# Kernel tuning notes

Measured on AMD Instinct MI355X. Metric: run time of the kernel, lower is better.

The kernel has to match this reference:

```python
import jax, jax.numpy as jnp
import numpy as np

N = 50000
E = 800000
NODE_DIM = 128
EDGE_DIM = 128
HIDDEN_DIM = 256


def setup_inputs() -> dict:
    key = jax.random.key(0)
    k_x, k_ei, k_ea, k_w1, k_b1, k_w2, k_b2 = jax.random.split(key, 7)
    x = jax.random.normal(k_x, (N, NODE_DIM), dtype=jnp.float32)
    edge_index = jax.random.randint(k_ei, (2, E), 0, N, dtype=jnp.int64)
    edge_attr = jax.random.normal(k_ea, (E, EDGE_DIM), dtype=jnp.float32)
    u = jnp.zeros((1, NODE_DIM), dtype=jnp.float32)
    batch = jnp.zeros((N,), dtype=jnp.int64)
    in_dim = NODE_DIM + EDGE_DIM
    # torch Linear: y = x @ W.T + b, W shaped [out, in]
    W1 = jax.random.normal(k_w1, (HIDDEN_DIM, in_dim), dtype=jnp.float32) / np.sqrt(in_dim)
    b1 = jax.random.normal(k_b1, (HIDDEN_DIM,), dtype=jnp.float32) * 0.01
    W2 = jax.random.normal(k_w2, (NODE_DIM, HIDDEN_DIM), dtype=jnp.float32) / np.sqrt(HIDDEN_DIM)
    b2 = jax.random.normal(k_b2, (NODE_DIM,), dtype=jnp.float32) * 0.01
    return {"x": x, "edge_index": edge_index, "edge_attr": edge_attr, "u": u,
            "batch": batch, "W1": W1, "b1": b1, "W2": W2, "b2": b2}


def reference(x, edge_index, edge_attr, u, batch, W1, b1, W2, b2):
    # row, col = edge_index; scatter_add edge features into destination nodes
    col = edge_index[1]
    agg = jax.ops.segment_sum(edge_attr, col, num_segments=x.shape[0])  # [N, EDGE_DIM]
    out = jnp.concatenate([x, agg], axis=1)                              # [N, NODE_DIM+EDGE_DIM]
    h = jax.nn.relu(out @ W1.T + b1)                                     # [N, HIDDEN_DIM]
    return h @ W2.T + b2                                                 # [N, NODE_DIM]
```

## Files before the change

### kernel.cpp

```cpp
#include <hip/hip_runtime.h>

typedef __bf16 bf16;
typedef __attribute__((ext_vector_type(8))) __bf16 bf16x8;
typedef __attribute__((ext_vector_type(4))) __bf16 bf16x4;
typedef __attribute__((ext_vector_type(4))) float f32x4;

#define ND 128
#define IN_DIM 256
#define HD 256
#define OUT_D 128
#define BCAP 128

__global__ __launch_bounds__(256) void prep_kernel(const float* __restrict__ W1,
                                                   const float* __restrict__ W2,
                                                   bf16* __restrict__ W1b,
                                                   bf16* __restrict__ W2b,
                                                   int* __restrict__ cnt, int N) {
    int i = blockIdx.x * 256 + threadIdx.x;
    if (i < HD * IN_DIM) W1b[i] = (bf16)W1[i];
    if (i < OUT_D * HD) W2b[i] = (bf16)W2[i];
    if (i < N) cnt[i] = 0;
}

__global__ __launch_bounds__(256) void bucket_kernel(const int* __restrict__ col,
                                                     int* __restrict__ cnt,
                                                     int* __restrict__ bucket, int E) {
    int e = blockIdx.x * blockDim.x + threadIdx.x;
    if (e < E) {
        int c = col[e];
        int slot = atomicAdd(&cnt[c], 1);
        if (slot < BCAP) bucket[(size_t)c * BCAP + slot] = e;
    }
}

__global__ __launch_bounds__(256) void gather_kernel(const float4* __restrict__ ea,
                                                     const float4* __restrict__ x,
                                                     const int* __restrict__ cnt,
                                                     const int* __restrict__ bucket,
                                                     bf16* __restrict__ rowb, int N) {
    int wave = (int)((blockIdx.x * (long long)blockDim.x + threadIdx.x) >> 6);
    int lane = threadIdx.x & 63;
    if (wave >= N) return;
    const int q = lane & 31;
    const int s = lane >> 5;

    if (s == 0) {
        float4 xv = x[wave * 32 + q];
        bf16x4 o;
        o[0] = (bf16)xv.x; o[1] = (bf16)xv.y; o[2] = (bf16)xv.z; o[3] = (bf16)xv.w;
        *(bf16x4*)(rowb + (size_t)wave * IN_DIM + q * 4) = o;
    }

    int deg = cnt[wave];
    if (deg > BCAP) deg = BCAP;
    const int* bl = bucket + (size_t)wave * BCAP;
    float4 acc = make_float4(0.f, 0.f, 0.f, 0.f);

    for (int chunk = 0; chunk < deg; chunk += 64) {
        const int c64 = min(64, deg - chunk);
        int myid = (chunk + lane < deg) ? bl[chunk + lane] : 0;
        int j0 = s, j1 = s + 2;
        int id0 = __shfl(myid, j0);
        int id1 = __shfl(myid, j1);
        float4 v0, v1;
        if (j0 < c64) v0 = ea[(id0 << 5) + q];
        if (j1 < c64) v1 = ea[(id1 << 5) + q];
        while (j0 < c64) {
            float4 c0 = v0;
            bool h1 = (j1 < c64);
            float4 c1;
            if (h1) c1 = v1;
            int j2 = j0 + 4, j3 = j1 + 4;
            int id2 = __shfl(myid, j2 & 63);
            int id3 = __shfl(myid, j3 & 63);
            if (j2 < c64) v0 = ea[(id2 << 5) + q];
            if (j3 < c64) v1 = ea[(id3 << 5) + q];
            acc.x += c0.x; acc.y += c0.y; acc.z += c0.z; acc.w += c0.w;
            if (h1) { acc.x += c1.x; acc.y += c1.y; acc.z += c1.z; acc.w += c1.w; }
            j0 = j2; j1 = j3;
        }
    }

    acc.x += __shfl_xor(acc.x, 32);
    acc.y += __shfl_xor(acc.y, 32);
    acc.z += __shfl_xor(acc.z, 32);
    acc.w += __shfl_xor(acc.w, 32);
    if (s == 0) {
        bf16x4 o;
        o[0] = (bf16)acc.x; o[1] = (bf16)acc.y; o[2] = (bf16)acc.z; o[3] = (bf16)acc.w;
        *(bf16x4*)(rowb + (size_t)wave * IN_DIM + ND + q * 4) = o;
    }
}

__device__ __forceinline__ int hswz(int row, int col) {
    int c = col >> 3, sub = col & 7;
    return row * HD + (((c ^ (row & 7)) << 3) | sub);
}

__global__ __launch_bounds__(256) void mlp_kernel(const bf16* __restrict__ rowb,
                                                  const bf16* __restrict__ W1b,
                                                  const float* __restrict__ b1,
                                                  const bf16* __restrict__ W2b,
                                                  const float* __restrict__ b2,
                                                  float* __restrict__ y, int N) {
    __shared__ bf16 hl[4][32 * HD];
    const int w = threadIdx.x >> 6;
    const int lane = threadIdx.x & 63;
    const int l15 = lane & 15;
    const int g = lane >> 4;
    const int nb0 = blockIdx.x * 128 + w * 32;
    const int nb1 = nb0 + 16;
    const bool val0 = nb0 < N, val1 = nb1 < N;
    const int nbe0 = val0 ? nb0 : 0;
    const int nbe1 = val1 ? nb1 : 0;

    bf16x8 a0[8], a1[8];
#pragma unroll
    for (int k0 = 0; k0 < 8; k0++) {
        a0[k0] = *(const bf16x8*)(rowb + (size_t)(nbe0 + l15) * IN_DIM + k0 * 32 + g * 8);
        a1[k0] = *(const bf16x8*)(rowb + (size_t)(nbe1 + l15) * IN_DIM + k0 * 32 + g * 8);
    }

#pragma unroll
    for (int jt = 0; jt < 16; jt++) {
        f32x4 acc0 = {0.f, 0.f, 0.f, 0.f}, acc1 = {0.f, 0.f, 0.f, 0.f};
#pragma unroll
        for (int k0 = 0; k0 < 8; k0++) {
            bf16x8 b = *(const bf16x8*)(W1b + (size_t)(jt * 16 + l15) * IN_DIM + k0 * 32 + g * 8);
            acc0 = __builtin_amdgcn_mfma_f32_16x16x32_bf16(a0[k0], b, acc0, 0, 0, 0);
            acc1 = __builtin_amdgcn_mfma_f32_16x16x32_bf16(a1[k0], b, acc1, 0, 0, 0);
        }
        float bj = b1[jt * 16 + l15];
        int colj = jt * 16 + l15;
#pragma unroll
        for (int r = 0; r < 4; r++) {
            int row = g * 4 + r;
            float v0 = acc0[r] + bj;
            float v1 = acc1[r] + bj;
            hl[w][hswz(row, colj)]      = (bf16)(v0 > 0.f ? v0 : 0.f);
            hl[w][hswz(row + 16, colj)] = (bf16)(v1 > 0.f ? v1 : 0.f);
        }
    }
    __syncthreads();

    bf16x8 h0[8], h1[8];
#pragma unroll
    for (int k0 = 0; k0 < 8; k0++) {
        h0[k0] = *(const bf16x8*)&hl[w][hswz(l15,      k0 * 32 + g * 8)];
        h1[k0] = *(const bf16x8*)&hl[w][hswz(l15 + 16, k0 * 32 + g * 8)];
    }

#pragma unroll
    for (int jt = 0; jt < 8; jt++) {
        f32x4 acc0 = {0.f, 0.f, 0.f, 0.f}, acc1 = {0.f, 0.f, 0.f, 0.f};
#pragma unroll
        for (int k0 = 0; k0 < 8; k0++) {
            bf16x8 b = *(const bf16x8*)(W2b + (size_t)(jt * 16 + l15) * HD + k0 * 32 + g * 8);
            acc0 = __builtin_amdgcn_mfma_f32_16x16x32_bf16(h0[k0], b, acc0, 0, 0, 0);
            acc1 = __builtin_amdgcn_mfma_f32_16x16x32_bf16(h1[k0], b, acc1, 0, 0, 0);
        }
        float bm = b2[jt * 16 + l15];
#pragma unroll
        for (int r = 0; r < 4; r++) {
            if (val0) y[(size_t)(nb0 + g * 4 + r) * OUT_D + jt * 16 + l15] = acc0[r] + bm;
            if (val1) y[(size_t)(nb1 + g * 4 + r) * OUT_D + jt * 16 + l15] = acc1[r] + bm;
        }
    }
}

extern "C" void kernel_launch(void* const* d_in, const int* in_sizes, int n_in,
                              void* d_out, int out_size, void* d_ws, size_t ws_size,
                              hipStream_t stream) {
    const float* x  = (const float*)d_in[0];
    const int* edge_index = (const int*)d_in[1];
    const float* ea = (const float*)d_in[2];
    const float* W1 = (const float*)d_in[5];
    const float* b1 = (const float*)d_in[6];
    const float* W2 = (const float*)d_in[7];
    const float* b2 = (const float*)d_in[8];
    float* y = (float*)d_out;

    const int E = in_sizes[1] / 2;
    const int N = in_sizes[0] / ND;
    const int* col = edge_index + E;

    char* ws = (char*)d_ws;
    size_t off = 0;
    bf16* rowb = (bf16*)(ws + off); off += (size_t)N * IN_DIM * sizeof(bf16);
    bf16* W1b  = (bf16*)(ws + off); off += (size_t)HD * IN_DIM * sizeof(bf16);
    bf16* W2b  = (bf16*)(ws + off); off += (size_t)OUT_D * HD * sizeof(bf16);
    int* cnt    = (int*)(ws + off); off += (size_t)N * sizeof(int);
    int* bucket = (int*)(ws + off); off += (size_t)N * BCAP * sizeof(int);

    prep_kernel<<<(HD * IN_DIM + 255) / 256, 256, 0, stream>>>(W1, W2, W1b, W2b, cnt, N);
    bucket_kernel<<<(E + 255) / 256, 256, 0, stream>>>(col, cnt, bucket, E);

    {
        long long threads = (long long)N * 64;
        int blocks = (int)((threads + 255) / 256);
        gather_kernel<<<blocks, 256, 0, stream>>>((const float4*)ea, (const float4*)x,
                                                  cnt, bucket, rowb, N);
    }

    mlp_kernel<<<(N + 127) / 128, 256, 0, stream>>>(rowb, W1b, b1, W2b, b2, y, N);
}
```

Measured before the change: 205.8 us.

## Fuse edge gather and MLP into one kernel with shared-memory row tile

New measurement: 244.5 us. +18.8%, slower.

```diff
diff --git a/kernel.cpp b/kernel.cpp
--- a/kernel.cpp
+++ b/kernel.cpp
@@ -10,6 +10,11 @@
 #define HD 256
 #define OUT_D 128
 #define BCAP 128
+
+__device__ __forceinline__ int hswz(int row, int col) {
+    int c = col >> 3, sub = col & 7;
+    return row * 256 + (((c ^ (row & 7)) << 3) | sub);
+}
 
 __global__ __launch_bounds__(256) void prep_kernel(const float* __restrict__ W1,
                                                    const float* __restrict__ W2,
@@ -33,137 +38,117 @@
     }
 }
 
-__global__ __launch_bounds__(256) void gather_kernel(const float4* __restrict__ ea,
-                                                     const float4* __restrict__ x,
-                                                     const int* __restrict__ cnt,
-                                                     const int* __restrict__ bucket,
-                                                     bf16* __restrict__ rowb, int N) {
-    int wave = (int)((blockIdx.x * (long long)blockDim.x + threadIdx.x) >> 6);
-    int lane = threadIdx.x & 63;
-    if (wave >= N) return;
+__global__ __launch_bounds__(256) void fused_kernel(const float4* __restrict__ ea,
+                                                    const float4* __restrict__ x,
+                                                    const int* __restrict__ cnt,
+                                                    const int* __restrict__ bucket,
+                                                    const bf16* __restrict__ W1b,
+                                                    const float* __restrict__ b1,
+                                                    const bf16* __restrict__ W2b,
+                                                    const float* __restrict__ b2,
+                                                    float* __restrict__ y, int N) {
+    __shared__ bf16 tile[64 * 256];
+    const int w = threadIdx.x >> 6;
+    const int lane = threadIdx.x & 63;
     const int q = lane & 31;
     const int s = lane >> 5;
+    const int l15 = lane & 15;
+    const int g = lane >> 4;
+    const int nb = blockIdx.x * 64 + w * 16;
+    const bool valid = nb < N;
 
-    if (s == 0) {
-        float4 xv = x[wave * 32 + q];
-        bf16x4 o;
-        o[0] = (bf16)xv.x; o[1] = (bf16)xv.y; o[2] = (bf16)xv.z; o[3] = (bf16)xv.w;
-        *(bf16x4*)(rowb + (size_t)wave * IN_DIM + q * 4) = o;
-    }
-
-    int deg = cnt[wave];
-    if (deg > BCAP) deg = BCAP;
-    const int* bl = bucket + (size_t)wave * BCAP;
-    float4 acc = make_float4(0.f, 0.f, 0.f, 0.f);
-
-    for (int chunk = 0; chunk < deg; chunk += 64) {
-        const int c64 = min(64, deg - chunk);
-        int myid = (chunk + lane < deg) ? bl[chunk + lane] : 0;
-        int j0 = s, j1 = s + 2;
-        int id0 = __shfl(myid, j0);
-        int id1 = __shfl(myid, j1);
-        float4 v0, v1;
-        if (j0 < c64) v0 = ea[(id0 << 5) + q];
-        if (j1 < c64) v1 = ea[(id1 << 5) + q];
-        while (j0 < c64) {
-            float4 c0 = v0;
-            bool h1 = (j1 < c64);
-            float4 c1;
-            if (h1) c1 = v1;
-            int j2 = j0 + 4, j3 = j1 + 4;
-            int id2 = __shfl(myid, j2 & 63);
-            int id3 = __shfl(myid, j3 & 63);
-            if (j2 < c64) v0 = ea[(id2 << 5) + q];
-            if (j3 < c64) v1 = ea[(id3 << 5) + q];
-            acc.x += c0.x; acc.y += c0.y; acc.z += c0.z; acc.w += c0.w;
-            if (h1) { acc.x += c1.x; acc.y += c1.y; acc.z += c1.z; acc.w += c1.w; }
-            j0 = j2; j1 = j3;
+    if (valid) {
+        for (int n = 0; n < 16; n++) {
+            const int nd = nb + n;
+            const int row = w * 16 + n;
+            if (s == 0) {
+                float4 xv = x[nd * 32 + q];
+                bf16x4 o;
+                o[0] = (bf16)xv.x; o[1] = (bf16)xv.y; o[2] = (bf16)xv.z; o[3] = (bf16)xv.w;
+                *(bf16x4*)&tile[hswz(row, q * 4)] = o;
+            }
+            int deg = cnt[nd]; if (deg > BCAP) deg = BCAP;
+            const int* bl = bucket + (size_t)nd * BCAP;
+            float4 acc = make_float4(0.f, 0.f, 0.f, 0.f);
+            for (int chunk = 0; chunk < deg; chunk += 64) {
+                const int c64 = min(64, deg - chunk);
+                int myid = (chunk + lane < deg) ? bl[chunk + lane] : 0;
+                int j0 = s, j1 = s + 2;
+                int id0 = __shfl(myid, j0);
+                int id1 = __shfl(myid, j1);
+                float4 v0, v1;
+                if (j0 < c64) v0 = ea[(id0 << 5) + q];
+                if (j1 < c64) v1 = ea[(id1 << 5) + q];
+                while (j0 < c64) {
+                    float4 c0 = v0;
+                    bool h1 = (j1 < c64);
+                    float4 c1; if (h1) c1 = v1;
+                    int j2 = j0 + 4, j3 = j1 + 4;
+                    int id2 = __shfl(myid, j2 & 63);
+                    int id3 = __shfl(myid, j3 & 63);
+                    if (j2 < c64) v0 = ea[(id2 << 5) + q];
+                    if (j3 < c64) v1 = ea[(id3 << 5) + q];
+                    acc.x += c0.x; acc.y += c0.y; acc.z += c0.z; acc.w += c0.w;
+                    if (h1) { acc.x += c1.x; acc.y += c1.y; acc.z += c1.z; acc.w += c1.w; }
+                    j0 = j2; j1 = j3;
+                }
+            }
+            acc.x += __shfl_xor(acc.x, 32);
+            acc.y += __shfl_xor(acc.y, 32);
+            acc.z += __shfl_xor(acc.z, 32);
+            acc.w += __shfl_xor(acc.w, 32);
+            if (s == 0) {
+                bf16x4 o;
+                o[0] = (bf16)acc.x; o[1] = (bf16)acc.y; o[2] = (bf16)acc.z; o[3] = (bf16)acc.w;
+                *(bf16x4*)&tile[hswz(row, ND + q * 4)] = o;
+            }
         }
     }
+    __syncthreads();
 
-    acc.x += __shfl_xor(acc.x, 32);
-    acc.y += __shfl_xor(acc.y, 32);
-    acc.z += __shfl_xor(acc.z, 32);
-    acc.w += __shfl_xor(acc.w, 32);
-    if (s == 0) {
-        bf16x4 o;
-        o[0] = (bf16)acc.x; o[1] = (bf16)acc.y; o[2] = (bf16)acc.z; o[3] = (bf16)acc.w;
-        *(bf16x4*)(rowb + (size_t)wave * IN_DIM + ND + q * 4) = o;
-    }
-}
-
-__device__ __forceinline__ int hswz(int row, int col) {
-    int c = col >> 3, sub = col & 7;
-    return row * HD + (((c ^ (row & 7)) << 3) | sub);
-}
-
-__global__ __launch_bounds__(256) void mlp_kernel(const bf16* __restrict__ rowb,
-                                                  const bf16* __restrict__ W1b,
-                                                  const float* __restrict__ b1,
-                                                  const bf16* __restrict__ W2b,
-                                                  const float* __restrict__ b2,
-                                                  float* __restrict__ y, int N) {
-    __shared__ bf16 hl[4][32 * HD];
-    const int w = threadIdx.x >> 6;
-    const int lane = threadIdx.x & 63;
-    const int l15 = lane & 15;
-    const int g = lane >> 4;
-    const int nb0 = blockIdx.x * 128 + w * 32;
-    const int nb1 = nb0 + 16;
-    const bool val0 = nb0 < N, val1 = nb1 < N;
-    const int nbe0 = val0 ? nb0 : 0;
-    const int nbe1 = val1 ? nb1 : 0;
-
-    bf16x8 a0[8], a1[8];
+    bf16x8 a[8];
 #pragma unroll
-    for (int k0 = 0; k0 < 8; k0++) {
-        a0[k0] = *(const bf16x8*)(rowb + (size_t)(nbe0 + l15) * IN_DIM + k0 * 32 + g * 8);
-        a1[k0] = *(const bf16x8*)(rowb + (size_t)(nbe1 + l15) * IN_DIM + k0 * 32 + g * 8);
-    }
+    for (int k0 = 0; k0 < 8; k0++)
+        a[k0] = *(const bf16x8*)&tile[hswz(w * 16 + l15, k0 * 32 + g * 8)];
+    __syncthreads();
 
 #pragma unroll
     for (int jt = 0; jt < 16; jt++) {
-        f32x4 acc0 = {0.f, 0.f, 0.f, 0.f}, acc1 = {0.f, 0.f, 0.f, 0.f};
+        f32x4 acc = {0.f, 0.f, 0.f, 0.f};
 #pragma unroll
         for (int k0 = 0; k0 < 8; k0++) {
             bf16x8 b = *(const bf16x8*)(W1b + (size_t)(jt * 16 + l15) * IN_DIM + k0 * 32 + g * 8);
-            acc0 = __builtin_amdgcn_mfma_f32_16x16x32_bf16(a0[k0], b, acc0, 0, 0, 0);
-            acc1 = __builtin_amdgcn_mfma_f32_16x16x32_bf16(a1[k0], b, acc1, 0, 0, 0);
+            acc = __builtin_amdgcn_mfma_f32_16x16x32_bf16(a[k0], b, acc, 0, 0, 0);
         }
         float bj = b1[jt * 16 + l15];
         int colj = jt * 16 + l15;
 #pragma unroll
         for (int r = 0; r < 4; r++) {
-            int row = g * 4 + r;
-            float v0 = acc0[r] + bj;
-            float v1 = acc1[r] + bj;
-            hl[w][hswz(row, colj)]      = (bf16)(v0 > 0.f ? v0 : 0.f);
-            hl[w][hswz(row + 16, colj)] = (bf16)(v1 > 0.f ? v1 : 0.f);
+            int row = w * 16 + g * 4 + r;
+            float v = acc[r] + bj;
+            tile[hswz(row, colj)] = (bf16)(v > 0.f ? v : 0.f);
         }
     }
     __syncthreads();
 
-    bf16x8 h0[8], h1[8];
+    bf16x8 h[8];
 #pragma unroll
-    for (int k0 = 0; k0 < 8; k0++) {
-        h0[k0] = *(const bf16x8*)&hl[w][hswz(l15,      k0 * 32 + g * 8)];
-        h1[k0] = *(const bf16x8*)&hl[w][hswz(l15 + 16, k0 * 32 + g * 8)];
-    }
+    for (int k0 = 0; k0 < 8; k0++)
+        h[k0] = *(const bf16x8*)&tile[hswz(w * 16 + l15, k0 * 32 + g * 8)];
 
 #pragma unroll
     for (int jt = 0; jt < 8; jt++) {
-        f32x4 acc0 = {0.f, 0.f, 0.f, 0.f}, acc1 = {0.f, 0.f, 0.f, 0.f};
+        f32x4 acc = {0.f, 0.f, 0.f, 0.f};
 #pragma unroll
         for (int k0 = 0; k0 < 8; k0++) {
             bf16x8 b = *(const bf16x8*)(W2b + (size_t)(jt * 16 + l15) * HD + k0 * 32 + g * 8);
-            acc0 = __builtin_amdgcn_mfma_f32_16x16x32_bf16(h0[k0], b, acc0, 0, 0, 0);
-            acc1 = __builtin_amdgcn_mfma_f32_16x16x32_bf16(h1[k0], b, acc1, 0, 0, 0);
+            acc = __builtin_amdgcn_mfma_f32_16x16x32_bf16(h[k0], b, acc, 0, 0, 0);
         }
         float bm = b2[jt * 16 + l15];
 #pragma unroll
         for (int r = 0; r < 4; r++) {
-            if (val0) y[(size_t)(nb0 + g * 4 + r) * OUT_D + jt * 16 + l15] = acc0[r] + bm;
-            if (val1) y[(size_t)(nb1 + g * 4 + r) * OUT_D + jt * 16 + l15] = acc1[r] + bm;
+            if (valid)
+                y[(size_t)(nb + g * 4 + r) * OUT_D + jt * 16 + l15] = acc[r] + bm;
         }
     }
 }
@@ -186,7 +171,6 @@
 
     char* ws = (char*)d_ws;
     size_t off = 0;
-    bf16* rowb = (bf16*)(ws + off); off += (size_t)N * IN_DIM * sizeof(bf16);
     bf16* W1b  = (bf16*)(ws + off); off += (size_t)HD * IN_DIM * sizeof(bf16);
     bf16* W2b  = (bf16*)(ws + off); off += (size_t)OUT_D * HD * sizeof(bf16);
     int* cnt    = (int*)(ws + off); off += (size_t)N * sizeof(int);
@@ -195,12 +179,6 @@
     prep_kernel<<<(HD * IN_DIM + 255) / 256, 256, 0, stream>>>(W1, W2, W1b, W2b, cnt, N);
     bucket_kernel<<<(E + 255) / 256, 256, 0, stream>>>(col, cnt, bucket, E);
 
-    {
-        long long threads = (long long)N * 64;
-        int blocks = (int)((threads + 255) / 256);
-        gather_kernel<<<blocks, 256, 0, stream>>>((const float4*)ea, (const float4*)x,
-                                                  cnt, bucket, rowb, N);
-    }
-
-    mlp_kernel<<<(N + 127) / 128, 256, 0, stream>>>(rowb, W1b, b1, W2b, b2, y, N);
+    fused_kernel<<<(N + 63) / 64, 256, 0, stream>>>((const float4*)ea, (const float4*)x,
+                                                    cnt, bucket, W1b, b1, W2b, b2, y, N);
 }
```
